# Kernel optimization log

Hardware: AMD Instinct MI355X
Metric: run time of the kernel (lower is better)

## Reference

```python
import jax, jax.numpy as jnp
import numpy as np

B, T, V, E, H, C = 128, 512, 100000, 100, 128, 3


def _lstm_dir(xs, w_ih, w_hh, b, reverse=False):
    # xs: [T,B,D]; w_ih: [4H,D]; w_hh: [4H,H]; b: [4H] (b_ih+b_hh combined)
    Tn, Bn, _ = xs.shape
    Hn = w_hh.shape[1]
    if reverse:
        xs = xs[::-1]
    gx = jnp.einsum('tbd,gd->tbg', xs, w_ih) + b  # [T,B,4H] input projections

    def step(carry, g_in):
        h, c = carry
        gates = g_in + h @ w_hh.T
        i, f, g, o = jnp.split(gates, 4, axis=-1)  # torch gate order i,f,g,o
        i = jax.nn.sigmoid(i)
        f = jax.nn.sigmoid(f)
        g = jnp.tanh(g)
        o = jax.nn.sigmoid(o)
        c = f * c + i * g
        h = o * jnp.tanh(c)
        return (h, c), h

    init = (jnp.zeros((Bn, Hn), xs.dtype), jnp.zeros((Bn, Hn), xs.dtype))
    (h_last, _), hs = jax.lax.scan(step, init, gx)
    if reverse:
        hs = hs[::-1]
    return hs, h_last


def setup_inputs() -> dict:
    key = jax.random.key(0)
    ks = jax.random.split(key, 24)
    s_e = 1.0 / np.sqrt(H)

    def u(k, shape):
        return jax.random.uniform(k, shape, jnp.float32, -s_e, s_e)

    x = jax.random.randint(ks[0], (B, T), 0, V, dtype=jnp.int32)
    emb = jax.random.normal(ks[1], (V, E), jnp.float32)
    emb = emb.at[0].set(0.0)  # padding_idx=0
    inp = {'x': x, 'emb': emb}
    names = []
    idx = 2
    for layer, din in ((0, E), (1, 2 * H)):
        for suf in ('', 'r'):
            inp[f'w_ih_l{layer}{suf}'] = u(ks[idx], (4 * H, din)); idx += 1
            inp[f'w_hh_l{layer}{suf}'] = u(ks[idx], (4 * H, H)); idx += 1
            inp[f'b_ih_l{layer}{suf}'] = u(ks[idx], (4 * H,)); idx += 1
            inp[f'b_hh_l{layer}{suf}'] = u(ks[idx], (4 * H,)); idx += 1
    s_f = 1.0 / np.sqrt(2 * H)
    inp['fc_w'] = jax.random.uniform(ks[22], (C, 2 * H), jnp.float32, -s_f, s_f)
    inp['fc_b'] = jax.random.uniform(ks[23], (C,), jnp.float32, -s_f, s_f)
    return inp


def reference(x, emb, w_ih_l0, w_hh_l0, b_ih_l0, b_hh_l0,
              w_ih_l0r, w_hh_l0r, b_ih_l0r, b_hh_l0r,
              w_ih_l1, w_hh_l1, b_ih_l1, b_hh_l1,
              w_ih_l1r, w_hh_l1r, b_ih_l1r, b_hh_l1r,
              fc_w, fc_b):
    # dropout is identity in eval mode
    xe = emb[x]                      # [B,T,E]
    xs = jnp.transpose(xe, (1, 0, 2))  # [T,B,E]
    # layer 0 bidirectional
    hf0, _ = _lstm_dir(xs, w_ih_l0, w_hh_l0, b_ih_l0 + b_hh_l0, reverse=False)
    hb0, _ = _lstm_dir(xs, w_ih_l0r, w_hh_l0r, b_ih_l0r + b_hh_l0r, reverse=True)
    x1 = jnp.concatenate([hf0, hb0], axis=-1)  # [T,B,2H]
    # layer 1 bidirectional; only final hidden states needed
    _, hF = _lstm_dir(x1, w_ih_l1, w_hh_l1, b_ih_l1 + b_hh_l1, reverse=False)
    _, hB = _lstm_dir(x1, w_ih_l1r, w_hh_l1r, b_ih_l1r + b_hh_l1r, reverse=True)
    out = jnp.concatenate([hF, hB], axis=1)  # [B,2H] == cat(hidden[-2], hidden[-1])
    return out @ fc_w.T + fc_b  # [B,C]
```

## Files before the change

kernel.cpp:

```cpp
#include <hip/hip_runtime.h>
#include <hip/hip_bf16.h>
#include <math.h>

#define TT 512
#define BB 128
#define EE 100
#define HH 128
#define G4 512
#define K1 256

typedef __attribute__((ext_vector_type(8))) short bf16x8;
typedef __attribute__((ext_vector_type(4))) float f32x4;

__device__ inline unsigned short bf16_rne(float v) {
    __hip_bfloat16 h = __float2bfloat16(v);
    return *reinterpret_cast<unsigned short*>(&h);
}

__device__ inline void gload16(const void* g, void* l) {
    __builtin_amdgcn_global_load_lds(
        (const __attribute__((address_space(1))) void*)g,
        (__attribute__((address_space(3))) void*)l, 16, 0, 0);
}

template<int CTRL>
__device__ inline float dppf(float x) {
    int r = __builtin_amdgcn_update_dpp(0, __float_as_int(x), CTRL, 0xF, 0xF, true);
    return __int_as_float(r);
}

__global__ void embed_cvt(const int* __restrict__ x, const float* __restrict__ emb,
                          unsigned short* __restrict__ xs2) {
    int row = blockIdx.x;
    int k = threadIdx.x;
    int b = row & 127, t = row >> 7;
    int tok = x[b * TT + t];
    float v = (k < EE) ? emb[(size_t)tok * EE + k] : 0.f;
    xs2[(size_t)row * 128 + k] = bf16_rne(v);
}

__global__ void wcvt(const float* __restrict__ src, int Kin, int Kp,
                     unsigned short* __restrict__ dst) {
    int n = blockIdx.x;
    int k = threadIdx.x;
    int j = n & 3;
    int gate = ((j & 1) << 1) | (j >> 1);
    int r = gate * 128 + (n >> 2);
    float v = (k < Kin) ? src[(size_t)r * Kin + k] : 0.f;
    dst[(size_t)n * Kp + k] = bf16_rne(v);
}

__global__ void bias_cat(const float* __restrict__ bihf, const float* __restrict__ bhhf,
                         const float* __restrict__ bihr, const float* __restrict__ bhhr,
                         float* __restrict__ dst) {
    int n = blockIdx.x * 256 + threadIdx.x;
    int d = n >> 9, m = n & 511;
    int j = m & 3;
    int gate = ((j & 1) << 1) | (j >> 1);
    int src = gate * 128 + (m >> 2);
    const float* a = d ? bihr : bihf;
    const float* c = d ? bhhr : bhhf;
    dst[n] = a[src] + c[src];
}

__global__ void whh_pack(const float* __restrict__ whh, float* __restrict__ dst) {
    int u = blockIdx.x;
    int k = threadIdx.x;
    float4 v;
    v.x = whh[((size_t)(0 * 128 + u)) * 128 + k];
    v.y = whh[((size_t)(1 * 128 + u)) * 128 + k];
    v.z = whh[((size_t)(2 * 128 + u)) * 128 + k];
    v.w = whh[((size_t)(3 * 128 + u)) * 128 + k];
    reinterpret_cast<float4*>(dst)[(size_t)u * 128 + k] = v;
}

template<int K2>
__global__ __launch_bounds__(256) void gemm_mfma(
    const unsigned short* __restrict__ A2,
    const unsigned short* __restrict__ W2cat,
    const float* __restrict__ biascat,
    float* __restrict__ Cf, float* __restrict__ Cr,
    int t_base)
{
    __shared__ bf16x8 As[1024];
    __shared__ bf16x8 Bs[1024];
    int tid = threadIdx.x;
    int s = blockIdx.y;
    int dir = blockIdx.x >> 2;
    int nBase = (blockIdx.x & 3) * 128;
    int t = dir ? (TT - 1 - t_base - s) : (t_base + s);
    float* C = dir ? Cr : Cf;
    const unsigned short* Abase = A2 + (size_t)t * BB * K2;
    const unsigned short* Wbase = W2cat + (size_t)(dir * 512 + nBase) * K2;
    int lane = tid & 63, wid = tid >> 6;
    int wr = wid >> 1, wc = wid & 1;
    int l15 = lane & 15, g = lane >> 4;

    f32x4 acc[4][4];
    const f32x4 z = {0.f, 0.f, 0.f, 0.f};
    #pragma unroll
    for (int i = 0; i < 4; ++i)
        #pragma unroll
        for (int j = 0; j < 4; ++j) acc[i][j] = z;

    for (int kt = 0; kt < K2 / 64; ++kt) {
        #pragma unroll
        for (int j = 0; j < 4; ++j) {
            int p = tid + j * 256;
            int row = p >> 3;
            int k16 = (p & 7) ^ (row & 7);
            size_t goff = (size_t)row * K2 + kt * 64 + k16 * 8;
            gload16(Abase + goff, &As[p]);
            gload16(Wbase + goff, &Bs[p]);
        }
        __syncthreads();
        #pragma unroll
        for (int ks = 0; ks < 2; ++ks) {
            bf16x8 af[4], bfr[4];
            #pragma unroll
            for (int i = 0; i < 4; ++i) {
                int arow = wr * 64 + i * 16 + l15;
                int abyte = arow * 128 + ((ks * 64 + g * 16) ^ ((arow & 7) << 4));
                af[i] = As[abyte >> 4];
                int brow = wc * 64 + i * 16 + l15;
                int bbyte = brow * 128 + ((ks * 64 + g * 16) ^ ((brow & 7) << 4));
                bfr[i] = Bs[bbyte >> 4];
            }
            #pragma unroll
            for (int i = 0; i < 4; ++i)
                #pragma unroll
                for (int j = 0; j < 4; ++j)
                    acc[i][j] = __builtin_amdgcn_mfma_f32_16x16x32_bf16(
                        af[i], bfr[j], acc[i][j], 0, 0, 0);
        }
        __syncthreads();
    }
    #pragma unroll
    for (int i = 0; i < 4; ++i) {
        size_t crow0 = (size_t)s * 128 + wr * 64 + i * 16 + g * 4;
        #pragma unroll
        for (int j = 0; j < 4; ++j) {
            int col = nBase + wc * 64 + j * 16 + l15;
            float bsum = biascat[dir * 512 + col];
            #pragma unroll
            for (int r = 0; r < 4; ++r)
                C[(crow0 + r) * G4 + col] = acc[i][j][r] + bsum;
        }
    }
}

__device__ inline float sig_fast(float z) {
    return __builtin_amdgcn_rcpf(1.f + __expf(-z));
}

__global__ __launch_bounds__(512, 2) void lstm_chunk(
    const float* __restrict__ gxf,
    const float* __restrict__ gxr,
    const float* __restrict__ wpkf,
    const float* __restrict__ wpkr,
    float* __restrict__ h_state,
    float* __restrict__ c_state,
    unsigned short* __restrict__ out_x1,
    int t_base, int TC)
{
    int blk = blockIdx.x;
    int dir = blk >> 7;
    int b   = blk & 127;
    const float* gx  = dir ? gxr : gxf;
    const float* wpk = dir ? wpkr : wpkf;
    int tid = threadIdx.x;
    int u = tid >> 2, q = tid & 3;

    const f32x4* wp4 = reinterpret_cast<const f32x4*>(wpk) + ((size_t)u * 128 + q * 32);
#define LW(i) const f32x4 w##i = wp4[i];
    LW(0)  LW(1)  LW(2)  LW(3)  LW(4)  LW(5)  LW(6)  LW(7)
    LW(8)  LW(9)  LW(10) LW(11) LW(12) LW(13) LW(14) LW(15)
    LW(16) LW(17) LW(18) LW(19) LW(20) LW(21) LW(22) LW(23)
    LW(24) LW(25) LW(26) LW(27) LW(28) LW(29) LW(30) LW(31)
#undef LW

    __shared__ float hb[2][160];
    int sbase = (dir * BB + b) * HH;
    int hslot = (u >> 5) * 40 + (u & 31);
    float c = c_state[sbase + u];
    float h = 0.f;
    if (q == 0) hb[0][hslot] = h_state[sbase + u];
    __syncthreads();

    const float* gxrow = gx + b * G4 + tid;
    float gin = gxrow[0];
    bool odd2 = (q & 2) != 0;
    float fq = (q == 1) ? 2.f : 1.f;
    float bq = (q == 1) ? -1.f : 0.f;

    for (int s = 0; s < TC; ++s) {
        int p = s & 1;
        int sn = (s + 1 < TC) ? s + 1 : s;
        float gin_next = gxrow[(size_t)sn * BB * G4];

        const float4* hb4 = reinterpret_cast<const float4*>(&hb[p][40 * q]);
        float4 hv0 = hb4[0], hv1 = hb4[1], hv2 = hb4[2], hv3 = hb4[3];
        float4 hv4 = hb4[4], hv5 = hb4[5], hv6 = hb4[6], hv7 = hb4[7];

        f32x4 a0 = {0.f,0.f,0.f,0.f}, a1 = {0.f,0.f,0.f,0.f};
        f32x4 a2 = {0.f,0.f,0.f,0.f}, a3 = {0.f,0.f,0.f,0.f};
#define FM(i0,i1,i2,i3,HV) { \
        f32x4 hh; \
        hh = f32x4{HV.x,HV.x,HV.x,HV.x}; a0 = __builtin_elementwise_fma(w##i0, hh, a0); \
        hh = f32x4{HV.y,HV.y,HV.y,HV.y}; a1 = __builtin_elementwise_fma(w##i1, hh, a1); \
        hh = f32x4{HV.z,HV.z,HV.z,HV.z}; a2 = __builtin_elementwise_fma(w##i2, hh, a2); \
        hh = f32x4{HV.w,HV.w,HV.w,HV.w}; a3 = __builtin_elementwise_fma(w##i3, hh, a3); }
        FM(0,1,2,3,hv0)    FM(4,5,6,7,hv1)    FM(8,9,10,11,hv2)  FM(12,13,14,15,hv3)
        FM(16,17,18,19,hv4) FM(20,21,22,23,hv5) FM(24,25,26,27,hv6) FM(28,29,30,31,hv7)
#undef FM
        f32x4 acc = (a0 + a1) + (a2 + a3);

        float xs = acc.x + dppf<0xB1>(acc.x);
        float ys = acc.y + dppf<0xB1>(acc.y);
        float zs = acc.z + dppf<0xB1>(acc.z);
        float ws = acc.w + dppf<0xB1>(acc.w);
        bool oddq = (q & 1) != 0;
        float sa = oddq ? zs : xs;
        float sb = oddq ? ws : ys;
        float sa2 = sa + dppf<0x4E>(sa);
        float sb2 = sb + dppf<0x4E>(sb);
        float pre_dot = odd2 ? sb2 : sa2;

        float pre = pre_dot + gin;
        float act = __builtin_fmaf(sig_fast(pre * fq), fq, bq);

        float ig = dppf<0x00>(act);
        float gg = dppf<0x55>(act);
        float fg = dppf<0xAA>(act);
        float og = dppf<0xFF>(act);

        c = fg * c + ig * gg;
        float th = __builtin_fmaf(2.f, sig_fast(2.f * c), -1.f);
        h = og * th;

        if (q == 0) {
            hb[p ^ 1][hslot] = h;
            if (out_x1) {
                int tg = dir ? (TT - 1 - (t_base + s)) : (t_base + s);
                out_x1[((size_t)tg * BB + b) * 256 + dir * HH + u] = bf16_rne(h);
            }
        }
        asm volatile("s_waitcnt lgkmcnt(0)" ::: "memory");
        __builtin_amdgcn_s_barrier();
        asm volatile("" ::: "memory");
        gin = gin_next;
    }
    if (q == 0) {
        h_state[sbase + u] = h;
        c_state[sbase + u] = c;
    }
}

__global__ void fc_kernel(const float* __restrict__ h_state,
                          const float* __restrict__ fc_w,
                          const float* __restrict__ fc_b,
                          float* __restrict__ out) {
    int tid = blockIdx.x * blockDim.x + threadIdx.x;
    if (tid >= BB * 3) return;
    int b = tid / 3;
    int c = tid % 3;
    float acc = 0.f;
    for (int j = 0; j < 256; ++j) {
        float v = (j < HH) ? h_state[((size_t)0 * BB + b) * HH + j]
                           : h_state[((size_t)1 * BB + b) * HH + (j - HH)];
        acc += v * fc_w[c * 256 + j];
    }
    out[b * 3 + c] = acc + fc_b[c];
}

extern "C" void kernel_launch(void* const* d_in, const int* in_sizes, int n_in,
                              void* d_out, int out_size, void* d_ws, size_t ws_size,
                              hipStream_t stream) {
    const int*   x        = (const int*)  d_in[0];
    const float* emb      = (const float*)d_in[1];
    const float* w_ih_l0  = (const float*)d_in[2];
    const float* w_hh_l0  = (const float*)d_in[3];
    const float* b_ih_l0  = (const float*)d_in[4];
    const float* b_hh_l0  = (const float*)d_in[5];
    const float* w_ih_l0r = (const float*)d_in[6];
    const float* w_hh_l0r = (const float*)d_in[7];
    const float* b_ih_l0r = (const float*)d_in[8];
    const float* b_hh_l0r = (const float*)d_in[9];
    const float* w_ih_l1  = (const float*)d_in[10];
    const float* w_hh_l1  = (const float*)d_in[11];
    const float* b_ih_l1  = (const float*)d_in[12];
    const float* b_hh_l1  = (const float*)d_in[13];
    const float* w_ih_l1r = (const float*)d_in[14];
    const float* w_hh_l1r = (const float*)d_in[15];
    const float* b_ih_l1r = (const float*)d_in[16];
    const float* b_hh_l1r = (const float*)d_in[17];
    const float* fc_w     = (const float*)d_in[18];
    const float* fc_b     = (const float*)d_in[19];
    float* out = (float*)d_out;
    (void)in_sizes; (void)n_in; (void)out_size;

    size_t xs2_b   = (size_t)TT * BB * 128 * 2;
    size_t x1_b    = (size_t)TT * BB * 256 * 2;
    size_t w2l0_b  = (size_t)512 * 128 * 2;
    size_t w2l1_b  = (size_t)512 * 256 * 2;
    size_t bias_b  = (size_t)1024 * 4;
    size_t wpk_b   = (size_t)128 * 128 * 4 * 4;
    size_t state_b = (size_t)2 * BB * HH * 4;
    size_t fixed = xs2_b + x1_b + 2 * w2l0_b + 2 * w2l1_b + 2 * bias_b
                 + 4 * wpk_b + 2 * state_b + 4096;
    int TC = 512;
    while (TC > 8) {
        size_t chunk2 = (size_t)TC * BB * G4 * 4 * 2;
        if (fixed + chunk2 <= ws_size) break;
        TC >>= 1;
    }
    char* ws = (char*)d_ws;
    size_t off = 0;
    unsigned short* xs2   = (unsigned short*)(ws + off); off += xs2_b;
    unsigned short* x1_2  = (unsigned short*)(ws + off); off += x1_b;
    unsigned short* w2l0f = (unsigned short*)(ws + off); off += w2l0_b;
    unsigned short* w2l0r = (unsigned short*)(ws + off); off += w2l0_b;
    unsigned short* w2l1f = (unsigned short*)(ws + off); off += w2l1_b;
    unsigned short* w2l1r = (unsigned short*)(ws + off); off += w2l1_b;
    float* biasl0  = (float*)(ws + off); off += bias_b;
    float* biasl1  = (float*)(ws + off); off += bias_b;
    float* wpk0f   = (float*)(ws + off); off += wpk_b;
    float* wpk0r   = (float*)(ws + off); off += wpk_b;
    float* wpk1f   = (float*)(ws + off); off += wpk_b;
    float* wpk1r   = (float*)(ws + off); off += wpk_b;
    float* h_state = (float*)(ws + off); off += state_b;
    float* c_state = (float*)(ws + off); off += state_b;
    float* gxf     = (float*)(ws + off); off += (size_t)TC * BB * G4 * 4;
    float* gxr     = (float*)(ws + off);

    int NC = TT / TC;
    dim3 ggrid(8, TC);

    embed_cvt<<<TT * BB, 128, 0, stream>>>(x, emb, xs2);
    wcvt<<<512, 128, 0, stream>>>(w_ih_l0,  EE, 128, w2l0f);
    wcvt<<<512, 128, 0, stream>>>(w_ih_l0r, EE, 128, w2l0r);
    wcvt<<<512, 256, 0, stream>>>(w_ih_l1,  K1, 256, w2l1f);
    wcvt<<<512, 256, 0, stream>>>(w_ih_l1r, K1, 256, w2l1r);
    bias_cat<<<4, 256, 0, stream>>>(b_ih_l0, b_hh_l0, b_ih_l0r, b_hh_l0r, biasl0);
    bias_cat<<<4, 256, 0, stream>>>(b_ih_l1, b_hh_l1, b_ih_l1r, b_hh_l1r, biasl1);
    whh_pack<<<128, 128, 0, stream>>>(w_hh_l0,  wpk0f);
    whh_pack<<<128, 128, 0, stream>>>(w_hh_l0r, wpk0r);
    whh_pack<<<128, 128, 0, stream>>>(w_hh_l1,  wpk1f);
    whh_pack<<<128, 128, 0, stream>>>(w_hh_l1r, wpk1r);

    hipMemsetAsync(h_state, 0, state_b, stream);
    hipMemsetAsync(c_state, 0, state_b, stream);
    for (int ci = 0; ci < NC; ++ci) {
        int t0 = ci * TC;
        gemm_mfma<128><<<ggrid, 256, 0, stream>>>(xs2, w2l0f, biasl0, gxf, gxr, t0);
        lstm_chunk<<<256, 512, 0, stream>>>(gxf, gxr, wpk0f, wpk0r,
                                            h_state, c_state, x1_2, t0, TC);
    }
    hipMemsetAsync(h_state, 0, state_b, stream);
    hipMemsetAsync(c_state, 0, state_b, stream);
    for (int ci = 0; ci < NC; ++ci) {
        int t0 = ci * TC;
        gemm_mfma<256><<<ggrid, 256, 0, stream>>>(x1_2, w2l1f, biasl1, gxf, gxr, t0);
        lstm_chunk<<<256, 512, 0, stream>>>(gxf, gxr, wpk1f, wpk1r,
                                            h_state, c_state, nullptr, t0, TC);
    }
    fc_kernel<<<2, 192, 0, stream>>>(h_state, fc_w, fc_b, out);
}
```

Before: 872.9 us.

## Share hidden-state reads via DPP lane rotation and batch setup kernels

The recurrent step now has each lane read only 8 hidden values from LDS instead of 32. It gets the remaining three slices from neighbouring lanes through DPP permutes, which needs a swizzled packing order for the recurrent weights. The small weight, bias and packing launches are merged into fewer kernels, and the state memsets are replaced by an init flag on the first chunk. This cuts LDS traffic and launch overhead on the serial path, at the cost of extra DPP instructions and a more intricate index mapping.

```diff
diff --git a/kernel.cpp b/kernel.cpp
--- a/kernel.cpp
+++ b/kernel.cpp
@@ -27,6 +27,13 @@
 __device__ inline float dppf(float x) {
     int r = __builtin_amdgcn_update_dpp(0, __float_as_int(x), CTRL, 0xF, 0xF, true);
     return __int_as_float(r);
+}
+template<int CTRL>
+__device__ inline float4 dpp4f(float4 v) {
+    float4 r;
+    r.x = dppf<CTRL>(v.x); r.y = dppf<CTRL>(v.y);
+    r.z = dppf<CTRL>(v.z); r.w = dppf<CTRL>(v.w);
+    return r;
 }
 
 __global__ void embed_cvt(const int* __restrict__ x, const float* __restrict__ emb,
@@ -39,8 +46,11 @@
     xs2[(size_t)row * 128 + k] = bf16_rne(v);
 }
 
-__global__ void wcvt(const float* __restrict__ src, int Kin, int Kp,
-                     unsigned short* __restrict__ dst) {
+__global__ void wcvt2(const float* __restrict__ srcf, const float* __restrict__ srcr,
+                      int Kin, int Kp,
+                      unsigned short* __restrict__ dstf, unsigned short* __restrict__ dstr) {
+    const float* src = blockIdx.y ? srcr : srcf;
+    unsigned short* dst = blockIdx.y ? dstr : dstf;
     int n = blockIdx.x;
     int k = threadIdx.x;
     int j = n & 3;
@@ -50,28 +60,38 @@
     dst[(size_t)n * Kp + k] = bf16_rne(v);
 }
 
-__global__ void bias_cat(const float* __restrict__ bihf, const float* __restrict__ bhhf,
-                         const float* __restrict__ bihr, const float* __restrict__ bhhr,
-                         float* __restrict__ dst) {
+__global__ void bias2(const float* __restrict__ bihf0, const float* __restrict__ bhhf0,
+                      const float* __restrict__ bihr0, const float* __restrict__ bhhr0,
+                      const float* __restrict__ bihf1, const float* __restrict__ bhhf1,
+                      const float* __restrict__ bihr1, const float* __restrict__ bhhr1,
+                      float* __restrict__ dst) {
     int n = blockIdx.x * 256 + threadIdx.x;
-    int d = n >> 9, m = n & 511;
+    int layer = n >> 10;
+    int d = (n >> 9) & 1, m = n & 511;
     int j = m & 3;
     int gate = ((j & 1) << 1) | (j >> 1);
     int src = gate * 128 + (m >> 2);
-    const float* a = d ? bihr : bihf;
-    const float* c = d ? bhhr : bhhf;
+    const float* a = layer ? (d ? bihr1 : bihf1) : (d ? bihr0 : bihf0);
+    const float* c = layer ? (d ? bhhr1 : bhhf1) : (d ? bhhr0 : bhhf0);
     dst[n] = a[src] + c[src];
 }
 
-__global__ void whh_pack(const float* __restrict__ whh, float* __restrict__ dst) {
+__global__ void whh_pack4(const float* __restrict__ w0f, const float* __restrict__ w0r,
+                          const float* __restrict__ w1f, const float* __restrict__ w1r,
+                          float* __restrict__ dstbase) {
+    int which = blockIdx.y;
+    const float* src = which == 0 ? w0f : which == 1 ? w0r : which == 2 ? w1f : w1r;
+    float* dst = dstbase + (size_t)which * 128 * 128 * 4;
     int u = blockIdx.x;
-    int k = threadIdx.x;
+    int t = threadIdx.x;
+    int q = t >> 5, m = (t >> 3) & 3, kk = t & 7;
+    int k = 32 * q + 8 * ((u & 3) ^ m) + kk;
     float4 v;
-    v.x = whh[((size_t)(0 * 128 + u)) * 128 + k];
-    v.y = whh[((size_t)(1 * 128 + u)) * 128 + k];
-    v.z = whh[((size_t)(2 * 128 + u)) * 128 + k];
-    v.w = whh[((size_t)(3 * 128 + u)) * 128 + k];
-    reinterpret_cast<float4*>(dst)[(size_t)u * 128 + k] = v;
+    v.x = src[((size_t)(0 * 128 + u)) * 128 + k];
+    v.y = src[((size_t)(1 * 128 + u)) * 128 + k];
+    v.z = src[((size_t)(2 * 128 + u)) * 128 + k];
+    v.w = src[((size_t)(3 * 128 + u)) * 128 + k];
+    reinterpret_cast<float4*>(dst)[(size_t)u * 128 + t] = v;
 }
 
 template<int K2>
@@ -161,7 +181,7 @@
     float* __restrict__ h_state,
     float* __restrict__ c_state,
     unsigned short* __restrict__ out_x1,
-    int t_base, int TC)
+    int t_base, int TC, int init)
 {
     int blk = blockIdx.x;
     int dir = blk >> 7;
@@ -169,7 +189,7 @@
     const float* gx  = dir ? gxr : gxf;
     const float* wpk = dir ? wpkr : wpkf;
     int tid = threadIdx.x;
-    int u = tid >> 2, q = tid & 3;
+    int u = tid >> 2, q = tid & 3, jj = u & 3;
 
     const f32x4* wp4 = reinterpret_cast<const f32x4*>(wpk) + ((size_t)u * 128 + q * 32);
 #define LW(i) const f32x4 w##i = wp4[i];
@@ -179,14 +199,15 @@
     LW(24) LW(25) LW(26) LW(27) LW(28) LW(29) LW(30) LW(31)
 #undef LW
 
-    __shared__ float hb[2][160];
+    __shared__ float hb[2][144];
     int sbase = (dir * BB + b) * HH;
-    int hslot = (u >> 5) * 40 + (u & 31);
-    float c = c_state[sbase + u];
-    float h = 0.f;
-    if (q == 0) hb[0][hslot] = h_state[sbase + u];
+    int hslot = (u >> 5) * 36 + (u & 31);
+    float c = init ? 0.f : c_state[sbase + u];
+    float h = init ? 0.f : h_state[sbase + u];
+    if (q == 0) hb[0][hslot] = h;
     __syncthreads();
 
+    int roff = 36 * q + 8 * jj;
     const float* gxrow = gx + b * G4 + tid;
     float gin = gxrow[0];
     bool odd2 = (q & 2) != 0;
@@ -198,21 +219,27 @@
         int sn = (s + 1 < TC) ? s + 1 : s;
         float gin_next = gxrow[(size_t)sn * BB * G4];
 
-        const float4* hb4 = reinterpret_cast<const float4*>(&hb[p][40 * q]);
-        float4 hv0 = hb4[0], hv1 = hb4[1], hv2 = hb4[2], hv3 = hb4[3];
-        float4 hv4 = hb4[4], hv5 = hb4[5], hv6 = hb4[6], hv7 = hb4[7];
+        const float4* hp = reinterpret_cast<const float4*>(&hb[p][roff]);
+        float4 hA = hp[0], hB = hp[1];
+        float4 c1A = dpp4f<0x1B>(dpp4f<0x141>(hA));
+        float4 c1B = dpp4f<0x1B>(dpp4f<0x141>(hB));
+        float4 c2A = dpp4f<0x128>(hA);
+        float4 c2B = dpp4f<0x128>(hB);
+        float4 c3A = dpp4f<0x128>(c1A);
+        float4 c3B = dpp4f<0x128>(c1B);
 
         f32x4 a0 = {0.f,0.f,0.f,0.f}, a1 = {0.f,0.f,0.f,0.f};
         f32x4 a2 = {0.f,0.f,0.f,0.f}, a3 = {0.f,0.f,0.f,0.f};
-#define FM(i0,i1,i2,i3,HV) { \
-        f32x4 hh; \
-        hh = f32x4{HV.x,HV.x,HV.x,HV.x}; a0 = __builtin_elementwise_fma(w##i0, hh, a0); \
-        hh = f32x4{HV.y,HV.y,HV.y,HV.y}; a1 = __builtin_elementwise_fma(w##i1, hh, a1); \
-        hh = f32x4{HV.z,HV.z,HV.z,HV.z}; a2 = __builtin_elementwise_fma(w##i2, hh, a2); \
-        hh = f32x4{HV.w,HV.w,HV.w,HV.w}; a3 = __builtin_elementwise_fma(w##i3, hh, a3); }
-        FM(0,1,2,3,hv0)    FM(4,5,6,7,hv1)    FM(8,9,10,11,hv2)  FM(12,13,14,15,hv3)
-        FM(16,17,18,19,hv4) FM(20,21,22,23,hv5) FM(24,25,26,27,hv6) FM(28,29,30,31,hv7)
-#undef FM
+#define FMA1(W, HV, A) A = __builtin_elementwise_fma(W, f32x4{HV, HV, HV, HV}, A)
+        FMA1(w0,  hA.x, a0);  FMA1(w1,  hA.y, a1);  FMA1(w2,  hA.z, a2);  FMA1(w3,  hA.w, a3);
+        FMA1(w4,  hB.x, a0);  FMA1(w5,  hB.y, a1);  FMA1(w6,  hB.z, a2);  FMA1(w7,  hB.w, a3);
+        FMA1(w8,  c1A.x, a0); FMA1(w9,  c1A.y, a1); FMA1(w10, c1A.z, a2); FMA1(w11, c1A.w, a3);
+        FMA1(w12, c1B.x, a0); FMA1(w13, c1B.y, a1); FMA1(w14, c1B.z, a2); FMA1(w15, c1B.w, a3);
+        FMA1(w16, c2A.x, a0); FMA1(w17, c2A.y, a1); FMA1(w18, c2A.z, a2); FMA1(w19, c2A.w, a3);
+        FMA1(w20, c2B.x, a0); FMA1(w21, c2B.y, a1); FMA1(w22, c2B.z, a2); FMA1(w23, c2B.w, a3);
+        FMA1(w24, c3A.x, a0); FMA1(w25, c3A.y, a1); FMA1(w26, c3A.z, a2); FMA1(w27, c3A.w, a3);
+        FMA1(w28, c3B.x, a0); FMA1(w29, c3B.y, a1); FMA1(w30, c3B.z, a2); FMA1(w31, c3B.w, a3);
+#undef FMA1
         f32x4 acc = (a0 + a1) + (a2 + a3);
 
         float xs = acc.x + dppf<0xB1>(acc.x);
@@ -332,37 +359,29 @@
     float* c_state = (float*)(ws + off); off += state_b;
     float* gxf     = (float*)(ws + off); off += (size_t)TC * BB * G4 * 4;
     float* gxr     = (float*)(ws + off);
+    (void)biasl1;
 
     int NC = TT / TC;
     dim3 ggrid(8, TC);
 
     embed_cvt<<<TT * BB, 128, 0, stream>>>(x, emb, xs2);
-    wcvt<<<512, 128, 0, stream>>>(w_ih_l0,  EE, 128, w2l0f);
-    wcvt<<<512, 128, 0, stream>>>(w_ih_l0r, EE, 128, w2l0r);
-    wcvt<<<512, 256, 0, stream>>>(w_ih_l1,  K1, 256, w2l1f);
-    wcvt<<<512, 256, 0, stream>>>(w_ih_l1r, K1, 256, w2l1r);
-    bias_cat<<<4, 256, 0, stream>>>(b_ih_l0, b_hh_l0, b_ih_l0r, b_hh_l0r, biasl0);
-    bias_cat<<<4, 256, 0, stream>>>(b_ih_l1, b_hh_l1, b_ih_l1r, b_hh_l1r, biasl1);
-    whh_pack<<<128, 128, 0, stream>>>(w_hh_l0,  wpk0f);
-    whh_pack<<<128, 128, 0, stream>>>(w_hh_l0r, wpk0r);
-    whh_pack<<<128, 128, 0, stream>>>(w_hh_l1,  wpk1f);
-    whh_pack<<<128, 128, 0, stream>>>(w_hh_l1r, wpk1r);
-
-    hipMemsetAsync(h_state, 0, state_b, stream);
-    hipMemsetAsync(c_state, 0, state_b, stream);
+    wcvt2<<<dim3(512, 2), 128, 0, stream>>>(w_ih_l0, w_ih_l0r, EE, 128, w2l0f, w2l0r);
+    wcvt2<<<dim3(512, 2), 256, 0, stream>>>(w_ih_l1, w_ih_l1r, K1, 256, w2l1f, w2l1r);
+    bias2<<<8, 256, 0, stream>>>(b_ih_l0, b_hh_l0, b_ih_l0r, b_hh_l0r,
+                                 b_ih_l1, b_hh_l1, b_ih_l1r, b_hh_l1r, biasl0);
+    whh_pack4<<<dim3(128, 4), 128, 0, stream>>>(w_hh_l0, w_hh_l0r, w_hh_l1, w_hh_l1r, wpk0f);
+
     for (int ci = 0; ci < NC; ++ci) {
         int t0 = ci * TC;
         gemm_mfma<128><<<ggrid, 256, 0, stream>>>(xs2, w2l0f, biasl0, gxf, gxr, t0);
         lstm_chunk<<<256, 512, 0, stream>>>(gxf, gxr, wpk0f, wpk0r,
-                                            h_state, c_state, x1_2, t0, TC);
-    }
-    hipMemsetAsync(h_state, 0, state_b, stream);
-    hipMemsetAsync(c_state, 0, state_b, stream);
+                                            h_state, c_state, x1_2, t0, TC, ci == 0);
+    }
     for (int ci = 0; ci < NC; ++ci) {
         int t0 = ci * TC;
         gemm_mfma<256><<<ggrid, 256, 0, stream>>>(x1_2, w2l1f, biasl1, gxf, gxr, t0);
         lstm_chunk<<<256, 512, 0, stream>>>(gxf, gxr, wpk1f, wpk1r,
-                                            h_state, c_state, nullptr, t0, TC);
+                                            h_state, c_state, nullptr, t0, TC, ci == 0);
     }
     fc_kernel<<<2, 192, 0, stream>>>(h_state, fc_w, fc_b, out);
 }
```

New measurement: 887.4 us. About the same (+1.7%).
